# Performance work log

Hardware: AMD Instinct MI355X
Metric: run time of the kernel (lower is better)

Reference implementation:

```python
import jax, jax.numpy as jnp
import numpy as np

N_NODES = 8192
HIDDEN = 256
HEADS = 4
HEAD_DIM = HIDDEN // HEADS
NUM_EDGES = 4096
NUM_INC = 65536
LN_EPS = 1e-5


def setup_inputs() -> dict:
    key = jax.random.key(0)
    ks = jax.random.split(key, 8)
    scale = HIDDEN ** -0.5
    return {
        "x": jax.random.normal(ks[0], (N_NODES, HIDDEN), jnp.float32),
        "node_idx": jax.random.randint(ks[1], (NUM_INC,), 0, N_NODES),
        "edge_idx": jax.random.randint(ks[2], (NUM_INC,), 0, NUM_EDGES),
        "W_w": jax.random.normal(ks[3], (HIDDEN, HIDDEN), jnp.float32) * scale,
        "W_b": jax.random.normal(ks[4], (HIDDEN,), jnp.float32) * 0.02,
        "edge_att": jax.random.normal(ks[5], (HEADS, HEAD_DIM), jnp.float32) * scale,
        "out_w": jax.random.normal(ks[6], (HIDDEN, HIDDEN), jnp.float32) * scale,
        "out_b": jax.random.normal(ks[7], (HIDDEN,), jnp.float32) * 0.02,
    }


def reference(x, node_idx, edge_idx, W_w, W_b, edge_att, out_w, out_b):
    n = x.shape[0]
    e = node_idx.shape[0]
    # x' = W(x), split into heads: [N, heads, head_dim]
    xw = (x @ W_w.T + W_b).reshape(n, HEADS, HEAD_DIM)
    feat = xw[node_idx]                                   # [E, heads, hd]
    logits = jnp.einsum("ehd,hd->eh", feat, edge_att)      # [E, heads]
    # segment softmax over nodes within each hyperedge, per head
    seg_max = jax.ops.segment_max(logits, edge_idx, num_segments=NUM_EDGES)
    p = jnp.exp(logits - seg_max[edge_idx])
    seg_sum = jax.ops.segment_sum(p, edge_idx, num_segments=NUM_EDGES)
    attn = p / seg_sum[edge_idx]                           # [E, heads]
    attn_mean = attn.mean(axis=1)                          # mean over heads, [E]
    # hyperedges with < 2 nodes are skipped in the original
    sizes = jax.ops.segment_sum(jnp.ones((e,), x.dtype), edge_idx, num_segments=NUM_EDGES)
    valid = sizes[edge_idx] >= 2.0
    attn_mean = jnp.where(valid, attn_mean, 0.0)
    # scatter-add attention-weighted ORIGINAL features back to nodes
    contrib = attn_mean[:, None] * x[node_idx]             # [E, H]
    out = jnp.zeros_like(x).at[node_idx].add(contrib)
    # degree normalization counts ALL incidences (including size-1 edges)
    counts = jnp.zeros((n,), x.dtype).at[node_idx].add(1.0)
    out = out / jnp.clip(counts, 1.0)[:, None]
    out = out @ out_w.T + out_b
    # fresh nn.LayerNorm => affine identity, biased variance, eps=1e-5
    mu = out.mean(-1, keepdims=True)
    var = ((out - mu) ** 2).mean(-1, keepdims=True)
    out = (out - mu) / jnp.sqrt(var + LN_EPS)
    # NxN pairwise attention accumulation: AW[i,j] = sum_e attn_i(e)*count_j(e), diag zeroed
    A = jnp.zeros((n, NUM_EDGES), x.dtype).at[node_idx, edge_idx].add(attn_mean)
    B = jnp.zeros((n, NUM_EDGES), x.dtype).at[node_idx, edge_idx].add(1.0)
    attention_weights = A @ B.T
    attention_weights = attention_weights.at[jnp.diag_indices(n)].set(0.0)
    return out, attention_weights
```

## Files before the change

### kernel.cpp

```cpp
#include <hip/hip_runtime.h>
#include <stdint.h>

#define N_NODES  8192
#define HIDDEN   256
#define HEADS    4
#define HEAD_DIM 64
#define NUM_EDGES 4096
#define NUM_INC  65536
#define LN_EPS   1e-5f

typedef unsigned int uint_t;


#define OFF_SEGSZ    0
#define OFF_NCNT     16384
#define OFF_NFILL    49152
#define OFF_EFILL    81920
#define ZERO_BYTES   98304
#define OFF_VKH      98304
#define OFF_BL       102400
#define OFF_LOGIT    102464
#define OFF_NPTR     233536
#define OFF_EPTR     266320
#define OFF_SEGSUM   282720
#define OFF_NINC     348256
#define OFF_EMEM     610400
#define OFF_ATTN     872544

__global__ __launch_bounds__(256) void k_zero(uint_t* __restrict__ w) {
    w[blockIdx.x * 256 + threadIdx.x] = 0u;
}

__global__ __launch_bounds__(256) void k_fold(const float* __restrict__ Ww,
                                              const float* __restrict__ Wb,
                                              const float* __restrict__ ea,
                                              float* __restrict__ vkhT,
                                              float* __restrict__ bl) {
    int k = threadIdx.x, h = blockIdx.x;
    float a = 0.f;
    for (int d = 0; d < HEAD_DIM; ++d)
        a += ea[h * HEAD_DIM + d] * Ww[(size_t)(h * HEAD_DIM + d) * HIDDEN + k];
    vkhT[h * HIDDEN + k] = a;
    if (k == 0) {
        float b = 0.f;
        for (int d = 0; d < HEAD_DIM; ++d)
            b += Wb[h * HEAD_DIM + d] * ea[h * HEAD_DIM + d];
        bl[h] = b;
    }
}

__global__ __launch_bounds__(256) void k_logits(const float* __restrict__ x,
                                                const float* __restrict__ vkhT,
                                                const float* __restrict__ bl,
                                                float* __restrict__ logit) {
    __shared__ __align__(16) float xs[32 * HIDDEN];
    __shared__ __align__(16) float vs[HEADS * HIDDEN];
    __shared__ float bls[HEADS];
    int t = threadIdx.x, b = blockIdx.x;
    float4* xsv = (float4*)xs;
    const float4* xg = (const float4*)(x + (size_t)b * 32 * HIDDEN);
    #pragma unroll
    for (int i = 0; i < 8; ++i) xsv[i * 256 + t] = xg[i * 256 + t];
    ((float4*)vs)[t] = ((const float4*)vkhT)[t];
    if (t < HEADS) bls[t] = bl[t];
    __syncthreads();
    if (t < 128) {
        int n = t >> 2, h = t & 3;
        const float4* xr = (const float4*)(xs + n * HIDDEN);
        const float4* vr = (const float4*)(vs + h * HIDDEN);
        float acc = bls[h];
        for (int k4 = 0; k4 < HIDDEN / 4; ++k4) {
            float4 xv = xr[k4], vv = vr[k4];
            acc += xv.x * vv.x + xv.y * vv.y + xv.z * vv.z + xv.w * vv.w;
        }
        logit[(b * 32 + n) * HEADS + h] = acc;
    }
}

__global__ void k_pass1(const int* __restrict__ node_idx, const int* __restrict__ edge_idx,
                        int* __restrict__ seg_size, int* __restrict__ node_cnt) {
    int i = blockIdx.x * 256 + threadIdx.x;
    atomicAdd(&seg_size[edge_idx[i]], 1);
    atomicAdd(&node_cnt[node_idx[i]], 1);
}

__global__ __launch_bounds__(256) void k_scan(const int* __restrict__ node_cnt, int* __restrict__ node_ptr,
                                              const int* __restrict__ seg_size, int* __restrict__ edge_ptr) {
    __shared__ int part[256];
    const int* cnt; int* ptr; int n;
    if (blockIdx.x == 0) { cnt = node_cnt; ptr = node_ptr; n = N_NODES; }
    else                 { cnt = seg_size; ptr = edge_ptr; n = NUM_EDGES; }
    int t = threadIdx.x, C = n / 256;
    int s = 0;
    for (int j = 0; j < C; ++j) s += cnt[t * C + j];
    part[t] = s;
    __syncthreads();
    if (t == 0) {
        int run = 0;
        for (int i = 0; i < 256; ++i) { int tmp = part[i]; part[i] = run; run += tmp; }
        ptr[n] = run;
    }
    __syncthreads();
    int run = part[t];
    for (int j = 0; j < C; ++j) { ptr[t * C + j] = run; run += cnt[t * C + j]; }
}

__global__ void k_fill(const int* __restrict__ node_idx, const int* __restrict__ edge_idx,
                       const int* __restrict__ node_ptr, const int* __restrict__ edge_ptr,
                       int* __restrict__ node_fill, int* __restrict__ edge_fill,
                       int* __restrict__ node_inc, int* __restrict__ edge_mem) {
    int i = blockIdx.x * 256 + threadIdx.x;
    int n = node_idx[i], e = edge_idx[i];
    int p = node_ptr[n] + atomicAdd(&node_fill[n], 1);
    node_inc[p] = i;
    int q = edge_ptr[e] + atomicAdd(&edge_fill[e], 1);
    edge_mem[q] = n;
}

__global__ __launch_bounds__(256) void k_seg(const int* __restrict__ edge_ptr,
                                             const int* __restrict__ edge_mem,
                                             const float* __restrict__ logit,
                                             float* __restrict__ seg_sum) {
    int e = blockIdx.x * 256 + threadIdx.x;
    int qb = edge_ptr[e], qe = edge_ptr[e + 1];
    float s0 = 0, s1 = 0, s2 = 0, s3 = 0;
    for (int q = qb; q < qe; ++q) {
        int j = edge_mem[q];
        s0 += __expf(logit[j * 4 + 0]);
        s1 += __expf(logit[j * 4 + 1]);
        s2 += __expf(logit[j * 4 + 2]);
        s3 += __expf(logit[j * 4 + 3]);
    }
    seg_sum[e * 4 + 0] = s0; seg_sum[e * 4 + 1] = s1;
    seg_sum[e * 4 + 2] = s2; seg_sum[e * 4 + 3] = s3;
}

__global__ void k_attn(const int* __restrict__ node_idx, const int* __restrict__ edge_idx,
                       const float* __restrict__ logit, const float* __restrict__ seg_sum,
                       const int* __restrict__ seg_size, float* __restrict__ attn) {
    int i = blockIdx.x * 256 + threadIdx.x;
    int e = edge_idx[i];
    float a = 0.f;
    if (seg_size[e] >= 2) {
        int n = node_idx[i];
        float s = 0.f;
        #pragma unroll
        for (int h = 0; h < HEADS; ++h)
            s += __expf(logit[n * HEADS + h]) / seg_sum[e * HEADS + h];
        a = 0.25f * s;
    }
    attn[i] = a;
}

__global__ __launch_bounds__(256) void k_out(const float* __restrict__ x,
                                             const int* __restrict__ node_ptr,
                                             const int* __restrict__ node_inc,
                                             const float* __restrict__ attn,
                                             const float* __restrict__ out_w,
                                             const float* __restrict__ out_b,
                                             float* __restrict__ out) {
    __shared__ __align__(16) float y[16][260];
    __shared__ float sr[16], mu_s[16], rs_s[16];
    int t = threadIdx.x;
    int R = blockIdx.x * 16;
    if (t < 16) {
        int n = R + t;
        int pb = node_ptr[n], pe = node_ptr[n + 1];
        float w = 0.f;
        for (int p = pb; p < pe; ++p) w += attn[node_inc[p]];
        int c = pe - pb; if (c < 1) c = 1;
        sr[t] = w / (float)c;
    }
    __syncthreads();
    #pragma unroll
    for (int r = 0; r < 16; ++r)
        y[r][t] = sr[r] * x[(size_t)(R + r) * HIDDEN + t];
    __syncthreads();
    float acc[16];
    float bias = out_b[t];
    #pragma unroll
    for (int r = 0; r < 16; ++r) acc[r] = bias;
    const float4* wr4 = (const float4*)(out_w + (size_t)t * HIDDEN);
    for (int j4 = 0; j4 < HIDDEN / 4; ++j4) {
        float4 wv = wr4[j4];
        #pragma unroll
        for (int r = 0; r < 16; ++r) {
            float4 yv = *(const float4*)&y[r][j4 * 4];
            acc[r] += yv.x * wv.x + yv.y * wv.y + yv.z * wv.z + yv.w * wv.w;
        }
    }
    __syncthreads();
    #pragma unroll
    for (int r = 0; r < 16; ++r) y[r][t] = acc[r];
    __syncthreads();
    if (t < 16) {
        float m = 0.f;
        for (int j = 0; j < HIDDEN; ++j) m += y[t][j];
        m *= (1.0f / HIDDEN);
        float s2 = 0.f;
        for (int j = 0; j < HIDDEN; ++j) { float d = y[t][j] - m; s2 += d * d; }
        mu_s[t] = m;
        rs_s[t] = rsqrtf(s2 * (1.0f / HIDDEN) + LN_EPS);
    }
    __syncthreads();
    #pragma unroll
    for (int r = 0; r < 16; ++r)
        out[(size_t)(R + r) * HIDDEN + t] = (y[r][t] - mu_s[r]) * rs_s[r];
}

__global__ __launch_bounds__(256) void k_aw(const float* __restrict__ attn,
                                            const int* __restrict__ node_ptr,
                                            const int* __restrict__ node_inc,
                                            const int* __restrict__ edge_ptr,
                                            const int* __restrict__ edge_mem,
                                            const int* __restrict__ edge_idx,
                                            float* __restrict__ AW) {
    __shared__ __align__(16) float row[N_NODES];
    int t = threadIdx.x, w = t >> 6, lane = t & 63;
    int i = blockIdx.x;
    float4* rowv = (float4*)row;
    #pragma unroll
    for (int c = 0; c < 8; ++c) rowv[c * 256 + t] = make_float4(0.f, 0.f, 0.f, 0.f);
    __syncthreads();
    int pb = node_ptr[i], pe = node_ptr[i + 1];
    for (int p = pb + w; p < pe; p += 4) {
        int m = node_inc[p];
        float a = attn[m];
        if (a != 0.f) {
            int e = edge_idx[m];
            int qb = edge_ptr[e], qe = edge_ptr[e + 1];
            for (int q = qb + lane; q < qe; q += 64)
                atomicAdd(&row[edge_mem[q]], a);
        }
    }
    __syncthreads();
    if (t == 0) row[i] = 0.f;
    __syncthreads();
    float4* dst = (float4*)(AW + (size_t)i * N_NODES);
    #pragma unroll
    for (int c = 0; c < 8; ++c) dst[c * 256 + t] = rowv[c * 256 + t];
}

extern "C" void kernel_launch(void* const* d_in, const int* in_sizes, int n_in,
                              void* d_out, int out_size, void* d_ws, size_t ws_size,
                              hipStream_t stream) {
    const float* x        = (const float*)d_in[0];
    const int*   node_idx = (const int*)d_in[1];
    const int*   edge_idx = (const int*)d_in[2];
    const float* Ww       = (const float*)d_in[3];
    const float* Wb       = (const float*)d_in[4];
    const float* ea       = (const float*)d_in[5];
    const float* ow       = (const float*)d_in[6];
    const float* ob       = (const float*)d_in[7];
    float* out0 = (float*)d_out;
    float* aw   = out0 + (size_t)N_NODES * HIDDEN;

    char* ws = (char*)d_ws;
    int*   seg_size  = (int*)(ws + OFF_SEGSZ);
    int*   node_cnt  = (int*)(ws + OFF_NCNT);
    int*   node_fill = (int*)(ws + OFF_NFILL);
    int*   edge_fill = (int*)(ws + OFF_EFILL);
    float* vkhT      = (float*)(ws + OFF_VKH);
    float* bl        = (float*)(ws + OFF_BL);
    float* logit     = (float*)(ws + OFF_LOGIT);
    int*   node_ptr  = (int*)(ws + OFF_NPTR);
    int*   edge_ptr  = (int*)(ws + OFF_EPTR);
    float* seg_sum   = (float*)(ws + OFF_SEGSUM);
    int*   node_inc  = (int*)(ws + OFF_NINC);
    int*   edge_mem  = (int*)(ws + OFF_EMEM);
    float* attn      = (float*)(ws + OFF_ATTN);

    k_zero<<<ZERO_BYTES / 4 / 256, 256, 0, stream>>>((uint_t*)ws);
    k_fold<<<HEADS, 256, 0, stream>>>(Ww, Wb, ea, vkhT, bl);
    k_logits<<<N_NODES / 32, 256, 0, stream>>>(x, vkhT, bl, logit);
    k_pass1<<<NUM_INC / 256, 256, 0, stream>>>(node_idx, edge_idx, seg_size, node_cnt);
    k_scan<<<2, 256, 0, stream>>>(node_cnt, node_ptr, seg_size, edge_ptr);
    k_fill<<<NUM_INC / 256, 256, 0, stream>>>(node_idx, edge_idx, node_ptr, edge_ptr,
                                              node_fill, edge_fill, node_inc, edge_mem);
    k_seg<<<NUM_EDGES / 256, 256, 0, stream>>>(edge_ptr, edge_mem, logit, seg_sum);
    k_attn<<<NUM_INC / 256, 256, 0, stream>>>(node_idx, edge_idx, logit, seg_sum, seg_size, attn);
    k_out<<<N_NODES / 16, 256, 0, stream>>>(x, node_ptr, node_inc, attn, ow, ob, out0);
    k_aw<<<N_NODES, 256, 0, stream>>>(attn, node_ptr, node_inc, edge_ptr, edge_mem, edge_idx, aw);
}
```

Before: 398.2 us.

## Pack per-incidence attention and edge ranges in node order; use nontemporal AW stores

Replaces the per-incidence attention kernel with one that walks incidences in node-sorted order. It writes a packed record of attention weight plus the hyperedge's member range, so k_out and k_aw read one contiguous 16-byte item instead of chasing node_inc, edge_idx and edge_ptr. The large AW output is written with nontemporal stores to avoid polluting cache. The workspace slot now holds 16-byte items instead of floats, which enlarges the workspace footprint.

```diff
diff --git a/kernel.cpp b/kernel.cpp
--- a/kernel.cpp
+++ b/kernel.cpp
@@ -10,6 +10,7 @@
 #define LN_EPS   1e-5f
 
 typedef unsigned int uint_t;
+typedef float __attribute__((ext_vector_type(4))) f4v;
 
 
 #define OFF_SEGSZ    0
@@ -25,7 +26,7 @@
 #define OFF_SEGSUM   282720
 #define OFF_NINC     348256
 #define OFF_EMEM     610400
-#define OFF_ATTN     872544
+#define OFF_ITEM     872544
 
 __global__ __launch_bounds__(256) void k_zero(uint_t* __restrict__ w) {
     w[blockIdx.x * 256 + threadIdx.x] = 0u;
@@ -135,27 +136,37 @@
     seg_sum[e * 4 + 2] = s2; seg_sum[e * 4 + 3] = s3;
 }
 
-__global__ void k_attn(const int* __restrict__ node_idx, const int* __restrict__ edge_idx,
-                       const float* __restrict__ logit, const float* __restrict__ seg_sum,
-                       const int* __restrict__ seg_size, float* __restrict__ attn) {
-    int i = blockIdx.x * 256 + threadIdx.x;
-    int e = edge_idx[i];
+__global__ __launch_bounds__(256) void k_pairs(const int* __restrict__ node_inc,
+                                               const int* __restrict__ node_idx,
+                                               const int* __restrict__ edge_idx,
+                                               const int* __restrict__ edge_ptr,
+                                               const float* __restrict__ logit,
+                                               const float* __restrict__ seg_sum,
+                                               float4* __restrict__ item) {
+    int p = blockIdx.x * 256 + threadIdx.x;
+    int m = node_inc[p];
+    int e = edge_idx[m];
+    int qb = edge_ptr[e], qe = edge_ptr[e + 1];
     float a = 0.f;
-    if (seg_size[e] >= 2) {
-        int n = node_idx[i];
+    if (qe - qb >= 2) {
+        int n = node_idx[m];
         float s = 0.f;
         #pragma unroll
         for (int h = 0; h < HEADS; ++h)
             s += __expf(logit[n * HEADS + h]) / seg_sum[e * HEADS + h];
         a = 0.25f * s;
     }
-    attn[i] = a;
+    float4 it;
+    it.x = a;
+    it.y = __int_as_float(qb);
+    it.z = __int_as_float(qe);
+    it.w = 0.f;
+    item[p] = it;
 }
 
 __global__ __launch_bounds__(256) void k_out(const float* __restrict__ x,
                                              const int* __restrict__ node_ptr,
-                                             const int* __restrict__ node_inc,
-                                             const float* __restrict__ attn,
+                                             const float4* __restrict__ item,
                                              const float* __restrict__ out_w,
                                              const float* __restrict__ out_b,
                                              float* __restrict__ out) {
@@ -167,7 +178,7 @@
         int n = R + t;
         int pb = node_ptr[n], pe = node_ptr[n + 1];
         float w = 0.f;
-        for (int p = pb; p < pe; ++p) w += attn[node_inc[p]];
+        for (int p = pb; p < pe; ++p) w += item[p].x;
         int c = pe - pb; if (c < 1) c = 1;
         sr[t] = w / (float)c;
     }
@@ -208,12 +219,9 @@
         out[(size_t)(R + r) * HIDDEN + t] = (y[r][t] - mu_s[r]) * rs_s[r];
 }
 
-__global__ __launch_bounds__(256) void k_aw(const float* __restrict__ attn,
+__global__ __launch_bounds__(256) void k_aw(const float4* __restrict__ item,
                                             const int* __restrict__ node_ptr,
-                                            const int* __restrict__ node_inc,
-                                            const int* __restrict__ edge_ptr,
                                             const int* __restrict__ edge_mem,
-                                            const int* __restrict__ edge_idx,
                                             float* __restrict__ AW) {
     __shared__ __align__(16) float row[N_NODES];
     int t = threadIdx.x, w = t >> 6, lane = t & 63;
@@ -224,11 +232,10 @@
     __syncthreads();
     int pb = node_ptr[i], pe = node_ptr[i + 1];
     for (int p = pb + w; p < pe; p += 4) {
-        int m = node_inc[p];
-        float a = attn[m];
+        float4 it = item[p];
+        float a = it.x;
         if (a != 0.f) {
-            int e = edge_idx[m];
-            int qb = edge_ptr[e], qe = edge_ptr[e + 1];
+            int qb = __float_as_int(it.y), qe = __float_as_int(it.z);
             for (int q = qb + lane; q < qe; q += 64)
                 atomicAdd(&row[edge_mem[q]], a);
         }
@@ -236,9 +243,11 @@
     __syncthreads();
     if (t == 0) row[i] = 0.f;
     __syncthreads();
-    float4* dst = (float4*)(AW + (size_t)i * N_NODES);
-    #pragma unroll
-    for (int c = 0; c < 8; ++c) dst[c * 256 + t] = rowv[c * 256 + t];
+    f4v* dst = (f4v*)(AW + (size_t)i * N_NODES);
+    const f4v* src = (const f4v*)row;
+    #pragma unroll
+    for (int c = 0; c < 8; ++c)
+        __builtin_nontemporal_store(src[c * 256 + t], &dst[c * 256 + t]);
 }
 
 extern "C" void kernel_launch(void* const* d_in, const int* in_sizes, int n_in,
@@ -256,19 +265,19 @@
     float* aw   = out0 + (size_t)N_NODES * HIDDEN;
 
     char* ws = (char*)d_ws;
-    int*   seg_size  = (int*)(ws + OFF_SEGSZ);
-    int*   node_cnt  = (int*)(ws + OFF_NCNT);
-    int*   node_fill = (int*)(ws + OFF_NFILL);
-    int*   edge_fill = (int*)(ws + OFF_EFILL);
-    float* vkhT      = (float*)(ws + OFF_VKH);
-    float* bl        = (float*)(ws + OFF_BL);
-    float* logit     = (float*)(ws + OFF_LOGIT);
-    int*   node_ptr  = (int*)(ws + OFF_NPTR);
-    int*   edge_ptr  = (int*)(ws + OFF_EPTR);
-    float* seg_sum   = (float*)(ws + OFF_SEGSUM);
-    int*   node_inc  = (int*)(ws + OFF_NINC);
-    int*   edge_mem  = (int*)(ws + OFF_EMEM);
-    float* attn      = (float*)(ws + OFF_ATTN);
+    int*    seg_size  = (int*)(ws + OFF_SEGSZ);
+    int*    node_cnt  = (int*)(ws + OFF_NCNT);
+    int*    node_fill = (int*)(ws + OFF_NFILL);
+    int*    edge_fill = (int*)(ws + OFF_EFILL);
+    float*  vkhT      = (float*)(ws + OFF_VKH);
+    float*  bl        = (float*)(ws + OFF_BL);
+    float*  logit     = (float*)(ws + OFF_LOGIT);
+    int*    node_ptr  = (int*)(ws + OFF_NPTR);
+    int*    edge_ptr  = (int*)(ws + OFF_EPTR);
+    float*  seg_sum   = (float*)(ws + OFF_SEGSUM);
+    int*    node_inc  = (int*)(ws + OFF_NINC);
+    int*    edge_mem  = (int*)(ws + OFF_EMEM);
+    float4* item      = (float4*)(ws + OFF_ITEM);
 
     k_zero<<<ZERO_BYTES / 4 / 256, 256, 0, stream>>>((uint_t*)ws);
     k_fold<<<HEADS, 256, 0, stream>>>(Ww, Wb, ea, vkhT, bl);
@@ -278,7 +287,8 @@
     k_fill<<<NUM_INC / 256, 256, 0, stream>>>(node_idx, edge_idx, node_ptr, edge_ptr,
                                               node_fill, edge_fill, node_inc, edge_mem);
     k_seg<<<NUM_EDGES / 256, 256, 0, stream>>>(edge_ptr, edge_mem, logit, seg_sum);
-    k_attn<<<NUM_INC / 256, 256, 0, stream>>>(node_idx, edge_idx, logit, seg_sum, seg_size, attn);
-    k_out<<<N_NODES / 16, 256, 0, stream>>>(x, node_ptr, node_inc, attn, ow, ob, out0);
-    k_aw<<<N_NODES, 256, 0, stream>>>(attn, node_ptr, node_inc, edge_ptr, edge_mem, edge_idx, aw);
-}
+    k_pairs<<<NUM_INC / 256, 256, 0, stream>>>(node_inc, node_idx, edge_idx, edge_ptr,
+                                               logit, seg_sum, item);
+    k_out<<<N_NODES / 16, 256, 0, stream>>>(x, node_ptr, item, ow, ob, out0);
+    k_aw<<<N_NODES, 256, 0, stream>>>(item, node_ptr, edge_mem, aw);
+}
```

Result: no change. 397.1 us (-0.3%).
